# Optimization experiments

Hardware: AMD Instinct MI355X
Metric: run time of the kernel (lower is better)

## Reference

```python
import jax, jax.numpy as jnp
import numpy as np

B, T, IN, H, OUT = 2048, 512, 6, 32, 64


def setup_inputs() -> dict:
    key = jax.random.key(0)
    ks = jax.random.split(key, 13)
    s_in = 1.0 / np.sqrt(H)  # torch LSTM/Linear default uniform bound
    u = lambda k, shape, s: jax.random.uniform(k, shape, jnp.float32, -s, s)
    return {
        "imu": jax.random.normal(ks[0], (B, T, IN), jnp.float32),
        # layer 0 (input_size=6)
        "w_ih0": u(ks[1], (4 * H, IN), s_in),
        "w_hh0": u(ks[2], (4 * H, H), s_in),
        "b_ih0": u(ks[3], (4 * H,), s_in),
        "b_hh0": u(ks[4], (4 * H,), s_in),
        # layer 1 (input_size=32)
        "w_ih1": u(ks[5], (4 * H, H), s_in),
        "w_hh1": u(ks[6], (4 * H, H), s_in),
        "b_ih1": u(ks[7], (4 * H,), s_in),
        "b_hh1": u(ks[8], (4 * H,), s_in),
        # heads
        "wf": u(ks[9], (OUT, H), s_in),
        "bf": u(ks[10], (OUT,), s_in),
        "wn": u(ks[11], (OUT, H), s_in),
        "bn": u(ks[12], (OUT,), s_in),
    }


def _lstm_layer(x, w_ih, w_hh, b_ih, b_hh):
    # x: [B, T, in] -> h sequence [B, T, H]; torch gate order: i, f, g, o
    b = x.shape[0]
    # precompute input contribution once: [B, T, 4H]
    gx = jnp.einsum("bti,gi->btg", x, w_ih) + b_ih + b_hh

    def step(carry, g_t):
        h, c = carry
        gates = g_t + h @ w_hh.T  # [B, 4H]
        i = jax.nn.sigmoid(gates[:, :H])
        f = jax.nn.sigmoid(gates[:, H:2 * H])
        g = jnp.tanh(gates[:, 2 * H:3 * H])
        o = jax.nn.sigmoid(gates[:, 3 * H:])
        c = f * c + i * g
        h = o * jnp.tanh(c)
        return (h, c), h

    h0 = jnp.zeros((b, H), x.dtype)
    (_, _), hs = jax.lax.scan(step, (h0, h0), jnp.swapaxes(gx, 0, 1))
    return jnp.swapaxes(hs, 0, 1)  # [B, T, H]


def reference(imu, w_ih0, w_hh0, b_ih0, b_hh0, w_ih1, w_hh1, b_ih1, b_hh1, wf, bf, wn, bn):
    h = _lstm_layer(imu, w_ih0, w_hh0, b_ih0, b_hh0)
    h = _lstm_layer(h, w_ih1, w_hh1, b_ih1, b_hh1)
    last = h[:, -1, :]  # [B, H]
    a_i = last @ wf.T + bf
    R_i = jnp.exp(last @ wn.T + bn)
    return (a_i, R_i)
```

## Files before the change

### kernel.cpp

```cpp
#include <hip/hip_runtime.h>
#include <hip/hip_bf16.h>

#define TT 512
#define BPB 8
#define NBLK (2048 / BPB)
#define OUTD 64

typedef __attribute__((ext_vector_type(8))) short short8;
typedef __attribute__((ext_vector_type(4))) float f32x4;

__device__ __forceinline__ short f2bf(float x) {
    union { float f; unsigned u; } v; v.f = x;
    unsigned r = (v.u + 0x7FFFu + ((v.u >> 16) & 1u)) >> 16;
    return (short)r;
}
__device__ __forceinline__ float sigm(float x) {
    return __builtin_amdgcn_rcpf(1.f + __expf(-x));
}
__device__ __forceinline__ float tanh_fast(float x) {
    return 2.f * sigm(2.f * x) - 1.f;
}

#define ACT_UPDATE(acc, c, hval)                                   \
    {                                                              \
        float gi = sigm((acc)[0]);                                 \
        float gf = sigm((acc)[1]);                                 \
        float gg = tanh_fast((acc)[2]);                            \
        float go = sigm((acc)[3]);                                 \
        (c) = gf * (c) + gi * gg;                                  \
        (hval) = go * tanh_fast((c));                              \
    }

#define MERGE(mg, a0, a1, colhi)                                   \
    {                                                              \
        _Pragma("unroll")                                          \
        for (int r = 0; r < 4; ++r) {                              \
            float s = __shfl_xor((a1)[r], 8);                      \
            (mg)[r] = (colhi) ? s : (a0)[r];                       \
        }                                                          \
    }

__global__ __launch_bounds__(512, 1) void lstm2_inlane_kernel(
    const float* __restrict__ imu,
    const float* __restrict__ w_ih0, const float* __restrict__ w_hh0,
    const float* __restrict__ b_ih0, const float* __restrict__ b_hh0,
    const float* __restrict__ w_ih1, const float* __restrict__ w_hh1,
    const float* __restrict__ b_ih1, const float* __restrict__ b_hh1,
    const float* __restrict__ wf, const float* __restrict__ bf,
    const float* __restrict__ wn, const float* __restrict__ bn,
    float* __restrict__ out)
{
    const int tid   = threadIdx.x;
    const int l     = tid & 63;
    const int w     = tid >> 6;
    const int layer = w >> 2;
    const int pair  = w & 3;
    const int col   = l & 15;
    const int kg    = l >> 4;
    const bool colhi = (col >= 8);
    const int batch  = col & 7;

    __shared__ __align__(16) short xfrag[TT + 2][8][8];
    __shared__ __align__(16) short h1f[2][16][40];
    __shared__ __align__(16) short h2f[2][16][40];
    __shared__ __align__(16) float lasth[16][36];

    {
        short* p1 = &h1f[0][0][0];
        short* p2 = &h2f[0][0][0];
        for (int i = tid; i < 2 * 16 * 40; i += 512) { p1[i] = 0; p2[i] = 0; }
    }

    {
        const int bg0 = blockIdx.x * BPB;
        for (int p = tid; p < BPB * TT; p += 512) {
            const int b = p >> 9;
            const int t = p & (TT - 1);
            const float* src = imu + ((size_t)(bg0 + b) * TT + t) * 6;
            float2 a0 = *(const float2*)(src);
            float2 a1 = *(const float2*)(src + 2);
            float2 a2 = *(const float2*)(src + 4);
            unsigned* dst = (unsigned*)&xfrag[t][b][0];
            dst[0] = (unsigned short)f2bf(a0.x) | ((unsigned)(unsigned short)f2bf(a0.y) << 16);
            dst[1] = (unsigned short)f2bf(a1.x) | ((unsigned)(unsigned short)f2bf(a1.y) << 16);
            dst[2] = (unsigned short)f2bf(a2.x) | ((unsigned)(unsigned short)f2bf(a2.y) << 16);
            dst[3] = 0u;
        }
    }

    const int t0 = pair * 2, t1 = t0 + 1;
    const int m  = col;
    const int G0 = (m & 3) * 32 + t0 * 4 + (m >> 2);
    const int G1 = (m & 3) * 32 + t1 * 4 + (m >> 2);
    const int u0 = pair * 8 + kg;
    const int u1 = u0 + 4;
    const int myunit = u0 + (colhi ? 4 : 0);

    short8 A00, A01, A10, A11;
    f32x4 bias0, bias1;
    if (layer == 0) {
        #pragma unroll
        for (int j = 0; j < 8; ++j) {
            A00[j] = (kg == 0 && j < 6) ? f2bf(w_ih0[G0 * 6 + j]) : (short)0;
            A10[j] = (kg == 0 && j < 6) ? f2bf(w_ih0[G1 * 6 + j]) : (short)0;
            A01[j] = f2bf(w_hh0[G0 * 32 + kg * 8 + j]);
            A11[j] = f2bf(w_hh0[G1 * 32 + kg * 8 + j]);
        }
        #pragma unroll
        for (int r = 0; r < 4; ++r) {
            bias0[r] = b_ih0[r * 32 + u0] + b_hh0[r * 32 + u0];
            bias1[r] = b_ih0[r * 32 + u1] + b_hh0[r * 32 + u1];
        }
    } else {
        #pragma unroll
        for (int j = 0; j < 8; ++j) {
            A00[j] = f2bf(w_ih1[G0 * 32 + kg * 8 + j]);
            A10[j] = f2bf(w_ih1[G1 * 32 + kg * 8 + j]);
            A01[j] = f2bf(w_hh1[G0 * 32 + kg * 8 + j]);
            A11[j] = f2bf(w_hh1[G1 * 32 + kg * 8 + j]);
        }
        #pragma unroll
        for (int r = 0; r < 4; ++r) {
            bias0[r] = b_ih1[r * 32 + u0] + b_hh1[r * 32 + u0];
            bias1[r] = b_ih1[r * 32 + u1] + b_hh1[r * 32 + u1];
        }
    }

    float c = 0.f;

    const int xb = l & 7;
    const short8* h1r0  = (const short8*)&h1f[0][col][kg * 8];
    const short8* h1r1  = (const short8*)&h1f[1][col][kg * 8];
    const short8* h2r0  = (const short8*)&h2f[0][col][kg * 8];
    const short8* h2r1  = (const short8*)&h2f[1][col][kg * 8];

    __syncthreads();

    short8 xv_cur;
    if (layer == 0) {
        short8 xv = *(const short8*)&xfrag[0][xb][0];
        f32x4 a0 = bias0, a1 = bias1;
        a0 = __builtin_amdgcn_mfma_f32_16x16x32_bf16(A00, xv, a0, 0, 0, 0);
        a1 = __builtin_amdgcn_mfma_f32_16x16x32_bf16(A10, xv, a1, 0, 0, 0);
        f32x4 mg;
        MERGE(mg, a0, a1, colhi);
        float h;
        ACT_UPDATE(mg, c, h);
        h1f[1][batch][myunit] = f2bf(h);
        xv_cur = *(const short8*)&xfrag[1][xb][0];
    }
    __syncthreads();

#define STEP(T, H1R, H2R, WP)                                                   \
    {                                                                           \
        if (layer == 0) {                                                       \
            short8 hv = *(H1R);                                                 \
            f32x4 a0 = bias0, a1 = bias1;                                       \
            a0 = __builtin_amdgcn_mfma_f32_16x16x32_bf16(A00, xv_cur, a0, 0, 0, 0); \
            a1 = __builtin_amdgcn_mfma_f32_16x16x32_bf16(A10, xv_cur, a1, 0, 0, 0); \
            a0 = __builtin_amdgcn_mfma_f32_16x16x32_bf16(A01, hv, a0, 0, 0, 0); \
            a1 = __builtin_amdgcn_mfma_f32_16x16x32_bf16(A11, hv, a1, 0, 0, 0); \
            f32x4 mg;                                                           \
            MERGE(mg, a0, a1, colhi);                                           \
            float h;                                                            \
            ACT_UPDATE(mg, c, h);                                               \
            h1f[WP][batch][myunit] = f2bf(h);                                   \
            xv_cur = *(const short8*)&xfrag[(T) + 2][xb][0];                    \
        } else {                                                                \
            short8 av = *(H1R);                                                 \
            short8 bv = *(H2R);                                                 \
            f32x4 a0 = bias0, a1 = bias1;                                       \
            a0 = __builtin_amdgcn_mfma_f32_16x16x32_bf16(A00, av, a0, 0, 0, 0); \
            a0 = __builtin_amdgcn_mfma_f32_16x16x32_bf16(A01, bv, a0, 0, 0, 0); \
            a1 = __builtin_amdgcn_mfma_f32_16x16x32_bf16(A10, av, a1, 0, 0, 0); \
            a1 = __builtin_amdgcn_mfma_f32_16x16x32_bf16(A11, bv, a1, 0, 0, 0); \
            f32x4 mg;                                                           \
            MERGE(mg, a0, a1, colhi);                                           \
            float h;                                                            \
            ACT_UPDATE(mg, c, h);                                               \
            h2f[WP][batch][myunit] = f2bf(h);                                   \
        }                                                                       \
        __syncthreads();                                                        \
    }

    #pragma unroll 1
    for (int t = 0; t < TT - 2; t += 2) {
        STEP(t,     h1r1, h2r1, 0)
        STEP(t + 1, h1r0, h2r0, 1)
    }
    STEP(TT - 2, h1r1, h2r1, 0)

    if (layer == 1) {
        short8 av = *h1r0;
        short8 bv = *h2r0;
        f32x4 a0 = bias0, a1 = bias1;
        a0 = __builtin_amdgcn_mfma_f32_16x16x32_bf16(A00, av, a0, 0, 0, 0);
        a0 = __builtin_amdgcn_mfma_f32_16x16x32_bf16(A01, bv, a0, 0, 0, 0);
        a1 = __builtin_amdgcn_mfma_f32_16x16x32_bf16(A10, av, a1, 0, 0, 0);
        a1 = __builtin_amdgcn_mfma_f32_16x16x32_bf16(A11, bv, a1, 0, 0, 0);
        f32x4 mg;
        MERGE(mg, a0, a1, colhi);
        float h;
        ACT_UPDATE(mg, c, h);
        lasth[batch][myunit] = h;
    }
    __syncthreads();

    {
        const int b = tid >> 6;
        const int o = tid & 63;
        float accF = bf[o], accN = bn[o];
        const float4* wf4 = (const float4*)(wf + o * 32);
        const float4* wn4 = (const float4*)(wn + o * 32);
        const float4* hv4 = (const float4*)&lasth[b][0];
        #pragma unroll
        for (int k = 0; k < 8; ++k) {
            float4 h4 = hv4[k];
            float4 f4 = wf4[k];
            float4 n4 = wn4[k];
            accF += f4.x * h4.x + f4.y * h4.y + f4.z * h4.z + f4.w * h4.w;
            accN += n4.x * h4.x + n4.y * h4.y + n4.z * h4.z + n4.w * h4.w;
        }
        const size_t bg = (size_t)blockIdx.x * BPB + b;
        out[bg * OUTD + o] = accF;
        out[(size_t)2048 * OUTD + bg * OUTD + o] = __expf(accN);
    }
}

extern "C" void kernel_launch(void* const* d_in, const int* in_sizes, int n_in,
                              void* d_out, int out_size, void* d_ws, size_t ws_size,
                              hipStream_t stream) {
    const float* imu   = (const float*)d_in[0];
    const float* w_ih0 = (const float*)d_in[1];
    const float* w_hh0 = (const float*)d_in[2];
    const float* b_ih0 = (const float*)d_in[3];
    const float* b_hh0 = (const float*)d_in[4];
    const float* w_ih1 = (const float*)d_in[5];
    const float* w_hh1 = (const float*)d_in[6];
    const float* b_ih1 = (const float*)d_in[7];
    const float* b_hh1 = (const float*)d_in[8];
    const float* wf    = (const float*)d_in[9];
    const float* bf    = (const float*)d_in[10];
    const float* wn    = (const float*)d_in[11];
    const float* bn    = (const float*)d_in[12];
    float* out = (float*)d_out;

    lstm2_inlane_kernel<<<dim3(NBLK), dim3(512), 0, stream>>>(
        imu, w_ih0, w_hh0, b_ih0, b_hh0,
        w_ih1, w_hh1, b_ih1, b_hh1,
        wf, bf, wn, bn, out);
}
```

Measured before the change: 174.2 us.

## Precompute next-step input MFMA off the recurrent critical path, use hardware bf16 convert

Layer-0 waves now compute the input-projection MFMAs for step t+1 after writing h for step t, leaving only the two recurrent MFMAs on the dependency chain after each barrier. The x fragments rotate through two registers with a one-step prefetch, and xfrag is padded with zeroed rows so the lookahead reads stay in bounds. The software round-to-nearest bf16 conversion is replaced by the v_cvt_pk_bf16_f32 instruction. Layer-1 MFMAs are reordered so the two accumulators interleave. Costs are a few extra registers and slightly more LDS.

```diff
diff --git a/kernel.cpp b/kernel.cpp
--- a/kernel.cpp
+++ b/kernel.cpp
@@ -12,6 +12,11 @@
 __device__ __forceinline__ short f2bf(float x) {
     union { float f; unsigned u; } v; v.f = x;
     unsigned r = (v.u + 0x7FFFu + ((v.u >> 16) & 1u)) >> 16;
+    return (short)r;
+}
+__device__ __forceinline__ short cvt_bf16(float x) {
+    unsigned r;
+    asm("v_cvt_pk_bf16_f32 %0, %1, %1" : "=v"(r) : "v"(x));
     return (short)r;
 }
 __device__ __forceinline__ float sigm(float x) {
@@ -60,7 +65,7 @@
     const bool colhi = (col >= 8);
     const int batch  = col & 7;
 
-    __shared__ __align__(16) short xfrag[TT + 2][8][8];
+    __shared__ __align__(16) short xfrag[TT + 4][8][8];
     __shared__ __align__(16) short h1f[2][16][40];
     __shared__ __align__(16) short h2f[2][16][40];
     __shared__ __align__(16) float lasth[16][36];
@@ -69,6 +74,8 @@
         short* p1 = &h1f[0][0][0];
         short* p2 = &h2f[0][0][0];
         for (int i = tid; i < 2 * 16 * 40; i += 512) { p1[i] = 0; p2[i] = 0; }
+        short* px = &xfrag[TT][0][0];
+        for (int i = tid; i < 4 * 64; i += 512) px[i] = 0;
     }
 
     {
@@ -136,67 +143,67 @@
 
     __syncthreads();
 
-    short8 xv_cur;
+    short8 xvE = (short8)0, xvO = (short8)0;
+    f32x4 xacc0 = bias0, xacc1 = bias1;
     if (layer == 0) {
         short8 xv = *(const short8*)&xfrag[0][xb][0];
-        f32x4 a0 = bias0, a1 = bias1;
-        a0 = __builtin_amdgcn_mfma_f32_16x16x32_bf16(A00, xv, a0, 0, 0, 0);
-        a1 = __builtin_amdgcn_mfma_f32_16x16x32_bf16(A10, xv, a1, 0, 0, 0);
+        f32x4 a0 = __builtin_amdgcn_mfma_f32_16x16x32_bf16(A00, xv, bias0, 0, 0, 0);
+        f32x4 a1 = __builtin_amdgcn_mfma_f32_16x16x32_bf16(A10, xv, bias1, 0, 0, 0);
         f32x4 mg;
         MERGE(mg, a0, a1, colhi);
         float h;
         ACT_UPDATE(mg, c, h);
-        h1f[1][batch][myunit] = f2bf(h);
-        xv_cur = *(const short8*)&xfrag[1][xb][0];
+        h1f[1][batch][myunit] = cvt_bf16(h);
+        short8 xv1 = *(const short8*)&xfrag[1][xb][0];
+        xacc0 = __builtin_amdgcn_mfma_f32_16x16x32_bf16(A00, xv1, bias0, 0, 0, 0);
+        xacc1 = __builtin_amdgcn_mfma_f32_16x16x32_bf16(A10, xv1, bias1, 0, 0, 0);
+        xvE = *(const short8*)&xfrag[2][xb][0];
     }
     __syncthreads();
 
-#define STEP(T, H1R, H2R, WP)                                                   \
+#define STEP(T, H1R, H2R, WP, XVC, XVL)                                         \
     {                                                                           \
         if (layer == 0) {                                                       \
             short8 hv = *(H1R);                                                 \
-            f32x4 a0 = bias0, a1 = bias1;                                       \
-            a0 = __builtin_amdgcn_mfma_f32_16x16x32_bf16(A00, xv_cur, a0, 0, 0, 0); \
-            a1 = __builtin_amdgcn_mfma_f32_16x16x32_bf16(A10, xv_cur, a1, 0, 0, 0); \
-            a0 = __builtin_amdgcn_mfma_f32_16x16x32_bf16(A01, hv, a0, 0, 0, 0); \
-            a1 = __builtin_amdgcn_mfma_f32_16x16x32_bf16(A11, hv, a1, 0, 0, 0); \
+            f32x4 a0 = __builtin_amdgcn_mfma_f32_16x16x32_bf16(A01, hv, xacc0, 0, 0, 0); \
+            f32x4 a1 = __builtin_amdgcn_mfma_f32_16x16x32_bf16(A11, hv, xacc1, 0, 0, 0); \
             f32x4 mg;                                                           \
             MERGE(mg, a0, a1, colhi);                                           \
             float h;                                                            \
             ACT_UPDATE(mg, c, h);                                               \
-            h1f[WP][batch][myunit] = f2bf(h);                                   \
-            xv_cur = *(const short8*)&xfrag[(T) + 2][xb][0];                    \
+            h1f[WP][batch][myunit] = cvt_bf16(h);                               \
+            xacc0 = __builtin_amdgcn_mfma_f32_16x16x32_bf16(A00, XVC, bias0, 0, 0, 0); \
+            xacc1 = __builtin_amdgcn_mfma_f32_16x16x32_bf16(A10, XVC, bias1, 0, 0, 0); \
+            XVL = *(const short8*)&xfrag[(T) + 3][xb][0];                       \
         } else {                                                                \
             short8 av = *(H1R);                                                 \
             short8 bv = *(H2R);                                                 \
-            f32x4 a0 = bias0, a1 = bias1;                                       \
-            a0 = __builtin_amdgcn_mfma_f32_16x16x32_bf16(A00, av, a0, 0, 0, 0); \
+            f32x4 a0 = __builtin_amdgcn_mfma_f32_16x16x32_bf16(A00, av, bias0, 0, 0, 0); \
+            f32x4 a1 = __builtin_amdgcn_mfma_f32_16x16x32_bf16(A10, av, bias1, 0, 0, 0); \
             a0 = __builtin_amdgcn_mfma_f32_16x16x32_bf16(A01, bv, a0, 0, 0, 0); \
-            a1 = __builtin_amdgcn_mfma_f32_16x16x32_bf16(A10, av, a1, 0, 0, 0); \
             a1 = __builtin_amdgcn_mfma_f32_16x16x32_bf16(A11, bv, a1, 0, 0, 0); \
             f32x4 mg;                                                           \
             MERGE(mg, a0, a1, colhi);                                           \
             float h;                                                            \
             ACT_UPDATE(mg, c, h);                                               \
-            h2f[WP][batch][myunit] = f2bf(h);                                   \
+            h2f[WP][batch][myunit] = cvt_bf16(h);                               \
         }                                                                       \
         __syncthreads();                                                        \
     }
 
     #pragma unroll 1
     for (int t = 0; t < TT - 2; t += 2) {
-        STEP(t,     h1r1, h2r1, 0)
-        STEP(t + 1, h1r0, h2r0, 1)
-    }
-    STEP(TT - 2, h1r1, h2r1, 0)
+        STEP(t,     h1r1, h2r1, 0, xvE, xvO)
+        STEP(t + 1, h1r0, h2r0, 1, xvO, xvE)
+    }
+    STEP(TT - 2, h1r1, h2r1, 0, xvE, xvO)
 
     if (layer == 1) {
         short8 av = *h1r0;
         short8 bv = *h2r0;
-        f32x4 a0 = bias0, a1 = bias1;
-        a0 = __builtin_amdgcn_mfma_f32_16x16x32_bf16(A00, av, a0, 0, 0, 0);
+        f32x4 a0 = __builtin_amdgcn_mfma_f32_16x16x32_bf16(A00, av, bias0, 0, 0, 0);
+        f32x4 a1 = __builtin_amdgcn_mfma_f32_16x16x32_bf16(A10, av, bias1, 0, 0, 0);
         a0 = __builtin_amdgcn_mfma_f32_16x16x32_bf16(A01, bv, a0, 0, 0, 0);
-        a1 = __builtin_amdgcn_mfma_f32_16x16x32_bf16(A10, av, a1, 0, 0, 0);
         a1 = __builtin_amdgcn_mfma_f32_16x16x32_bf16(A11, bv, a1, 0, 0, 0);
         f32x4 mg;
         MERGE(mg, a0, a1, colhi);
```

Result: no change. 173.9 us (-0.2%).
